# Optimization experiments

Measured on AMD Instinct MI355X. Metric: run time of the kernel, lower is better.

Reference implementation:

```python
import jax, jax.numpy as jnp
import numpy as np

D_MODEL = 1024
RANK = 256
INIT_ALPHA = 0.5


def setup_inputs() -> dict:
    key = jax.random.key(0)
    ks = jax.random.split(key, 12)
    D, R = D_MODEL, RANK
    s = 0.02
    return {
        "x": jax.random.normal(ks[0], (4, 2048, D), dtype=jnp.float32),
        "Wq": jax.random.normal(ks[1], (D, D), dtype=jnp.float32) * s,
        "Wk": jax.random.normal(ks[2], (D, D), dtype=jnp.float32) * s,
        "Wo": jax.random.normal(ks[3], (D, D), dtype=jnp.float32) * s,
        "U_b": jax.random.normal(ks[4], (D, R), dtype=jnp.float32) * s,
        "V_b": jax.random.normal(ks[5], (D, R), dtype=jnp.float32) * s,
        "W_b": jax.random.normal(ks[6], (D, R), dtype=jnp.float32) * s,
        "bias_b": jnp.zeros((D,), dtype=jnp.float32),
        "U_t": jax.random.normal(ks[7], (D, R), dtype=jnp.float32) * s,
        "V_t": jax.random.normal(ks[8], (D, R), dtype=jnp.float32) * s,
        "W_t": jax.random.normal(ks[9], (D, R), dtype=jnp.float32) * s,
        "X_t": jax.random.normal(ks[10], (D, R), dtype=jnp.float32) * s,
        "bias_t": jnp.zeros((D,), dtype=jnp.float32),
        "alpha": jnp.asarray(INIT_ALPHA, dtype=jnp.float32),
    }


def reference(x, Wq, Wk, Wo, U_b, V_b, W_b, bias_b, U_t, V_t, W_t, X_t, bias_t, alpha):
    # Math identical to the original O(T^2 D) materialization (attention_mask=None path),
    # reduced to causal cumulative sums: sum_{j<=i} (q_i * k_j) = q_i * cumsum_j(k_j).
    B, T, D = x.shape
    Q = x @ Wq.T                      # [B,T,D] (nn.Linear: x @ W^T)
    K = x @ Wk.T
    counts = jnp.arange(1, T + 1, dtype=x.dtype)[None, :, None]  # [1,T,1]
    Z = jnp.cumsum(x, axis=1) / counts  # causal cumulative mean [B,T,D]

    # Bilinear: sum_{j<=i} ((Q_i V_b) * (K_j W_b)) U_b^T + bias_b (per j)
    a_b = Q @ V_b                     # [B,T,R]
    c_b = jnp.cumsum(K @ W_b, axis=1) # [B,T,R] causal sum over j
    bil = (a_b * c_b) @ U_b.T         # [B,T,D]

    # Trilinear: sum_{j<=i} ((Q_i V_t) * (K_j W_t) * (Z_i X_t)) U_t^T + bias_t
    a_t = Q @ V_t
    c_t = jnp.cumsum(K @ W_t, axis=1)
    z_t = Z @ X_t
    tri = (a_t * z_t * c_t) @ U_t.T   # [B,T,D]

    # Per-i division by n_valid = i+1; the per-(i,j) biases average back to themselves.
    out = (bil + alpha * tri) / counts + (bias_b + alpha * bias_t)
    return out @ Wo.T                 # W_O (dropout=0 -> identity)
```

## Files before the change

kernel.cpp:

```cpp
#include <hip/hip_runtime.h>

#define NBATCH  4
#define TSEQ    2048
#define MROWS   8192
#define NCAT    1280
#define NE      512

#define OFF_WQT   0u
#define OFF_WKT   524288u
#define OFF_WOB   1048576u
#define OFF_VCT   1572864u
#define OFF_WCT   1835008u
#define OFF_UCT   2097152u
#define OFF_B2    2359296u
#define OFF_PB    2360320u
#define OFF_GB    3015680u
#define OFF_Y     3277824u
#define OFF_SCR   13763584u
#define OFF_XB    13861888u
#define OFF_EB    OFF_XB

typedef __attribute__((ext_vector_type(8))) short bf16x8;
typedef __attribute__((ext_vector_type(4))) float f32x4;

__device__ __forceinline__ unsigned short f2bf(float f) {
  union { float f; unsigned u; } v; v.f = f;
  return (unsigned short)((v.u + 0x7fff + ((v.u >> 16) & 1)) >> 16);
}

__device__ __forceinline__ void gload16(const void* g, void* l) {
  __builtin_amdgcn_global_load_lds(
      (const __attribute__((address_space(1))) unsigned*)g,
      (__attribute__((address_space(3))) unsigned*)l, 16, 0, 0);
}

template <int EPI, int OBF, int CS>
__device__ __forceinline__ void mfma_tile(
    const short* __restrict__ A, const short* __restrict__ B, void* __restrict__ Cv,
    int K, int ldA, int ldB, int ldC, int m0, int n0,
    const float* __restrict__ bias, float* __restrict__ scr, short* L) {
  const int tid = threadIdx.x;
  const int l = tid & 63;
  const int wv = tid >> 6;
  const int wm = (wv >> 1) * 64, wn = (wv & 1) * 64;
  const int sr = tid >> 2;
  const int sc4 = tid & 3;
  const int arow = wm + (l & 15), brow = wn + (l & 15);
  const int kq = l >> 4;

  f32x4 acc[4][4] = {};

#define STAGE(k0, par) do {                                                  \
    short* As_ = L + (par) * 8192;                                           \
    short* Bs_ = As_ + 4096;                                                 \
    _Pragma("unroll")                                                        \
    for (int p = 0; p < 2; ++p) {                                            \
      const int r = p * 64 + sr;                                             \
      const int sw = (sc4 ^ (r & 3)) * 8;                                    \
      gload16(A + (size_t)(m0 + r) * ldA + (k0) + sw, As_ + r * 32 + sc4 * 8); \
      gload16(B + (size_t)(n0 + r) * ldB + (k0) + sw, Bs_ + r * 32 + sc4 * 8); \
    }                                                                        \
  } while (0)

#define COMPUTE(par) do {                                                    \
    short* As_ = L + (par) * 8192;                                           \
    short* Bs_ = As_ + 4096;                                                 \
    bf16x8 af[4], bfr[4];                                                    \
    _Pragma("unroll")                                                        \
    for (int m = 0; m < 4; ++m) {                                            \
      const int r = arow + m * 16;                                           \
      af[m] = *(const bf16x8*)&As_[r * 32 + ((kq ^ (r & 3)) * 8)];           \
    }                                                                        \
    _Pragma("unroll")                                                        \
    for (int n = 0; n < 4; ++n) {                                            \
      const int r = brow + n * 16;                                           \
      bfr[n] = *(const bf16x8*)&Bs_[r * 32 + ((kq ^ (r & 3)) * 8)];          \
    }                                                                        \
    _Pragma("unroll")                                                        \
    for (int m = 0; m < 4; ++m)                                              \
      _Pragma("unroll")                                                      \
      for (int n = 0; n < 4; ++n)                                            \
        acc[m][n] = __builtin_amdgcn_mfma_f32_16x16x32_bf16(af[m], bfr[n], acc[m][n], 0, 0, 0); \
  } while (0)

  STAGE(0, 0);
  const int nt = K >> 5;
  for (int t = 0; t < nt; ++t) {
    if (t + 1 < nt) {
      STAGE((t + 1) << 5, (t + 1) & 1);
      asm volatile("s_waitcnt vmcnt(4)" ::: "memory");
    } else {
      asm volatile("s_waitcnt vmcnt(0)" ::: "memory");
    }
    asm volatile("s_barrier" ::: "memory");
    COMPUTE(t & 1);
    asm volatile("s_barrier" ::: "memory");
  }
#undef STAGE
#undef COMPUTE

  const int cc = wn + (l & 15);
  const int crb = wm + (l >> 4) * 4;
#pragma unroll
  for (int m = 0; m < 4; ++m) {
#pragma unroll
    for (int j = 0; j < 4; ++j) {
      const int gm = m0 + crb + m * 16 + j;
      float inv = 1.0f;
      if (EPI) inv = 1.0f / (float)((gm & (TSEQ - 1)) + 1);
#pragma unroll
      for (int n = 0; n < 4; ++n) {
        const int gn = n0 + cc + n * 16;
        float v = acc[m][n][j];
        if (EPI) v = v * inv + bias[gn];
        if (OBF) ((short*)Cv)[(size_t)gm * ldC + gn] = (short)f2bf(v);
        else     ((float*)Cv)[(size_t)gm * ldC + gn] = v;
      }
    }
  }
  if (CS && n0 >= 512) {
    const int bb = (m0 + wm) >> 11;
    const int seg = ((m0 + wm) & (TSEQ - 1)) >> 6;
    float* sp = scr + (size_t)(bb * 32 + seg) * 768 + (n0 - 512);
#pragma unroll
    for (int n = 0; n < 4; ++n) {
      float s = 0.f;
#pragma unroll
      for (int m = 0; m < 4; ++m)
#pragma unroll
        for (int j = 0; j < 4; ++j) s += acc[m][n][j];
      s += __shfl_xor(s, 16, 64);
      s += __shfl_xor(s, 32, 64);
      if (l < 16) sp[cc + n * 16] = s;
    }
  }
}

__device__ __forceinline__ void xcd_swizzle(int& bx, int& by) {
  const int gx = gridDim.x;
  const int nwg = gx * gridDim.y;
  const int n = by * gx + bx;
  const int q = nwg >> 3;
  const int s = (n & 7) * q + (n >> 3);
  bx = s % gx; by = s / gx;
}

template <int EPI, int CS>
__global__ __launch_bounds__(256) void mfma_nt(
    const short* __restrict__ A, const short* __restrict__ B,
    float* __restrict__ C, int K, int ldA, int ldB, int ldC,
    const float* __restrict__ bias, float* __restrict__ scr) {
  __shared__ short L[16384];
  int bx = blockIdx.x, by = blockIdx.y;
  xcd_swizzle(bx, by);
  mfma_tile<EPI, 0, CS>(A, B, C, K, ldA, ldB, ldC,
                        by * 128, bx * 128, bias, scr, L);
}

__global__ __launch_bounds__(256) void prep_mfma(
    const short* __restrict__ VCT, const short* __restrict__ WQT,
    const short* __restrict__ WCT, const short* __restrict__ WKT,
    const short* __restrict__ WOB, const short* __restrict__ UCT,
    short* __restrict__ Pb, short* __restrict__ Gb) {
  __shared__ short L[16384];
  const int g = blockIdx.x >> 5, t = blockIdx.x & 31;
  if (g == 0)
    mfma_tile<0, 1, 0>(VCT, WQT, Pb, 1024, 1024, 1024, 1024,
                       (t >> 3) * 128, (t & 7) * 128, nullptr, nullptr, L);
  else if (g == 1)
    mfma_tile<0, 1, 0>(WCT, WKT, Pb + (size_t)512 * 1024, 1024, 1024, 1024, 1024,
                       (t >> 3) * 128, (t & 7) * 128, nullptr, nullptr, L);
  else
    mfma_tile<0, 1, 0>(WOB, UCT, Gb, 1024, 1024, 1024, 512,
                       (t >> 2) * 128, (t & 3) * 128, nullptr, nullptr, L);
}

__global__ __launch_bounds__(256) void prep_all(
    const float* __restrict__ Vb, const float* __restrict__ Vt,
    const float* __restrict__ Wb, const float* __restrict__ Wt,
    const float* __restrict__ Ub, const float* __restrict__ Ut,
    const float* __restrict__ Xt, const float* __restrict__ Wq,
    const float* __restrict__ Wk, const float* __restrict__ Wo,
    const float* __restrict__ x,
    const float* __restrict__ bias_b, const float* __restrict__ bias_t,
    const float* __restrict__ alpha_p,
    short* __restrict__ VCT, short* __restrict__ WCT, short* __restrict__ UCT,
    short* __restrict__ PbXt, short* __restrict__ WQT, short* __restrict__ WKT,
    short* __restrict__ WOB, short* __restrict__ xb, float* __restrict__ b2) {
  const int bid = blockIdx.x;
  const int tid = threadIdx.x;
  if (bid >= 10176) {
    const float al = *alpha_p;
    const int d = bid - 10176;
    float s = 0.f;
    for (int e = tid; e < 1024; e += 256)
      s += Wo[(size_t)d * 1024 + e] * (bias_b[e] + al * bias_t[e]);
    __shared__ float red[256];
    red[tid] = s; __syncthreads();
    for (int off = 128; off > 0; off >>= 1) {
      if (tid < off) red[tid] += red[tid + off];
      __syncthreads();
    }
    if (tid == 0) b2[d] = red[0];
    return;
  }
  if (bid >= 960) {
    const size_t j = ((size_t)(bid - 960) * 256 + tid) * 4;
    const int isWo = j < 1048576u;
    const float* s = isWo ? &Wo[j] : &x[j - 1048576u];
    const float4 v = *(const float4*)s;
    ushort4 o;
    o.x = f2bf(v.x); o.y = f2bf(v.y); o.z = f2bf(v.z); o.w = f2bf(v.w);
    unsigned short* dst = (unsigned short*)(isWo ? WOB : xb);
    *(ushort4*)&dst[isWo ? j : j - 1048576u] = o;
    return;
  }
  const float* src; short* O; int r0, d0, c0, ldS;
  if (bid < 384) {
    const int z = bid >> 7, t = bid & 127;
    r0 = (t >> 4) * 64; d0 = (t & 15) * 64; ldS = 256;
    const float* S0 = z == 0 ? Vb : z == 1 ? Wb : Ub;
    const float* S1 = z == 0 ? Vt : z == 1 ? Wt : Ut;
    O = z == 0 ? VCT : z == 1 ? WCT : UCT;
    src = (r0 < 256) ? S0 : S1; c0 = r0 & 255;
  } else if (bid < 448) {
    const int t = bid - 384;
    r0 = (t >> 4) * 64; d0 = (t & 15) * 64; ldS = 256;
    src = Xt; c0 = r0; O = PbXt;
  } else {
    const int t = bid - 448;
    const int w = t >> 8, tt = t & 255;
    r0 = (tt >> 4) * 64; d0 = (tt & 15) * 64; ldS = 1024;
    src = w ? Wk : Wq; O = w ? WKT : WQT; c0 = r0;
  }
  __shared__ float Ts[64][65];
  const int lr = tid >> 4;
  const int lc = (tid & 15) * 4;
#pragma unroll
  for (int p = 0; p < 4; ++p) {
    const int row = lr + p * 16;
    const float4 v = *(const float4*)&src[(size_t)(d0 + row) * ldS + c0 + lc];
    Ts[row][lc + 0] = v.x; Ts[row][lc + 1] = v.y;
    Ts[row][lc + 2] = v.z; Ts[row][lc + 3] = v.w;
  }
  __syncthreads();
#pragma unroll
  for (int p = 0; p < 4; ++p) {
    const int ri = lr + p * 16;
    ushort4 o;
    o.x = f2bf(Ts[lc + 0][ri]); o.y = f2bf(Ts[lc + 1][ri]);
    o.z = f2bf(Ts[lc + 2][ri]); o.w = f2bf(Ts[lc + 3][ri]);
    *(ushort4*)&((unsigned short*)O)[(size_t)(r0 + ri) * 1024 + d0 + lc] = o;
  }
}

__global__ void cumsum_s2(float* __restrict__ scr) {
  const int lane = threadIdx.x;
  const int cg = blockIdx.x, b = blockIdx.z;
  const int c = cg * 64 + lane;
  float run = 0.f;
  for (int seg = 0; seg < 32; ++seg) {
    const size_t idx = (size_t)(b * 32 + seg) * 768 + c;
    const float v = scr[idx];
    scr[idx] = run;
    run += v;
  }
}

__global__ __launch_bounds__(256) void scan_combine(
    const float* __restrict__ Y, const float* __restrict__ scr,
    short* __restrict__ Eb, const float* __restrict__ alpha_p) {
  const float al = *alpha_p;
  const int c2 = threadIdx.x;
  const int seg = blockIdx.x, b = blockIdx.y;
  const float* sc = scr + (size_t)(b * 32 + seg) * 768;
  float run_cb = sc[c2];
  float run_ct = sc[256 + c2];
  float run_zt = sc[512 + c2];
  const size_t row0 = (size_t)(b * TSEQ + seg * 64);
  const float* yr = Y + row0 * NCAT;
  float ab = yr[c2], at = yr[256 + c2];
  float cb = yr[512 + c2], ct = yr[768 + c2], zt = yr[1024 + c2];
  for (int tt = 0; tt < 64; ++tt) {
    float nab = 0, nat = 0, ncb = 0, nct = 0, nzt = 0;
    if (tt < 63) {
      const float* yn = yr + NCAT;
      nab = yn[c2]; nat = yn[256 + c2];
      ncb = yn[512 + c2]; nct = yn[768 + c2]; nzt = yn[1024 + c2];
    }
    run_cb += cb; run_ct += ct; run_zt += zt;
    const float inv = 1.0f / (float)(seg * 64 + tt + 1);
    short* er = Eb + (row0 + tt) * 512;
    er[c2]       = (short)f2bf(ab * run_cb);
    er[256 + c2] = (short)f2bf(al * at * (run_zt * inv) * run_ct);
    ab = nab; at = nat; cb = ncb; ct = nct; zt = nzt;
    yr += NCAT;
  }
}

extern "C" void kernel_launch(void* const* d_in, const int* in_sizes, int n_in,
                              void* d_out, int out_size, void* d_ws, size_t ws_size,
                              hipStream_t stream) {
  const float* x      = (const float*)d_in[0];
  const float* Wq     = (const float*)d_in[1];
  const float* Wk     = (const float*)d_in[2];
  const float* Wo     = (const float*)d_in[3];
  const float* Ub     = (const float*)d_in[4];
  const float* Vb     = (const float*)d_in[5];
  const float* Wb     = (const float*)d_in[6];
  const float* bias_b = (const float*)d_in[7];
  const float* Ut     = (const float*)d_in[8];
  const float* Vt     = (const float*)d_in[9];
  const float* Wt     = (const float*)d_in[10];
  const float* Xt     = (const float*)d_in[11];
  const float* bias_t = (const float*)d_in[12];
  const float* alpha  = (const float*)d_in[13];
  float* out = (float*)d_out;
  float* ws  = (float*)d_ws;

  short* WQT = (short*)(ws + OFF_WQT);
  short* WKT = (short*)(ws + OFF_WKT);
  short* WOB = (short*)(ws + OFF_WOB);
  short* VCT = (short*)(ws + OFF_VCT);
  short* WCT = (short*)(ws + OFF_WCT);
  short* UCT = (short*)(ws + OFF_UCT);
  float* b2  = ws + OFF_B2;
  short* Pb  = (short*)(ws + OFF_PB);
  short* Gb  = (short*)(ws + OFF_GB);
  float* Y   = ws + OFF_Y;
  float* scr = ws + OFF_SCR;
  short* xb  = (short*)(ws + OFF_XB);
  short* Eb  = (short*)(ws + OFF_EB);

  prep_all<<<11200, 256, 0, stream>>>(Vb, Vt, Wb, Wt, Ub, Ut, Xt, Wq, Wk, Wo, x,
                                      bias_b, bias_t, alpha,
                                      VCT, WCT, UCT, Pb + (size_t)1024 * 1024,
                                      WQT, WKT, WOB, xb, b2);
  prep_mfma<<<96, 256, 0, stream>>>(VCT, WQT, WCT, WKT, WOB, UCT, Pb, Gb);
  mfma_nt<0, 1><<<dim3(NCAT / 128, MROWS / 128), 256, 0, stream>>>(
      xb, Pb, Y, 1024, 1024, 1024, NCAT, nullptr, scr);
  cumsum_s2<<<dim3(12, 1, NBATCH), 64, 0, stream>>>(scr);
  scan_combine<<<dim3(32, NBATCH), 256, 0, stream>>>(Y, scr, Eb, alpha);
  mfma_nt<1, 0><<<dim3(1024 / 128, MROWS / 128), 256, 0, stream>>>(
      Eb, Gb, out, 512, 512, 512, 1024, b2, nullptr);
}
```

Measured before the change: 203.3 us.

## Triple-buffer GEMM LDS pipeline, store Y in bf16, unroll scan with prefetch

The shared MFMA tile loop moves from double to triple buffering in LDS, so global loads run two k-steps ahead. The first GEMM now writes its intermediate Y in bf16 rather than fp32, which halves that write and the matching read in scan_combine. scan_combine is unrolled eight rows deep with register prefetch to hide load latency in the serial scan. The costs are 50% more LDS per block, which may lower occupancy, and extra rounding error from storing Y in bf16 before the cumulative sums.

```diff
diff --git a/kernel.cpp b/kernel.cpp
--- a/kernel.cpp
+++ b/kernel.cpp
@@ -27,6 +27,10 @@
   union { float f; unsigned u; } v; v.f = f;
   return (unsigned short)((v.u + 0x7fff + ((v.u >> 16) & 1)) >> 16);
 }
+__device__ __forceinline__ float bf2f(unsigned short u) {
+  union { unsigned u; float f; } v; v.u = ((unsigned)u) << 16;
+  return v.f;
+}
 
 __device__ __forceinline__ void gload16(const void* g, void* l) {
   __builtin_amdgcn_global_load_lds(
@@ -50,8 +54,8 @@
 
   f32x4 acc[4][4] = {};
 
-#define STAGE(k0, par) do {                                                  \
-    short* As_ = L + (par) * 8192;                                           \
+#define STAGE(k0, buf) do {                                                  \
+    short* As_ = L + (buf) * 8192;                                           \
     short* Bs_ = As_ + 4096;                                                 \
     _Pragma("unroll")                                                        \
     for (int p = 0; p < 2; ++p) {                                            \
@@ -62,8 +66,8 @@
     }                                                                        \
   } while (0)
 
-#define COMPUTE(par) do {                                                    \
-    short* As_ = L + (par) * 8192;                                           \
+#define COMPUTE(buf) do {                                                    \
+    short* As_ = L + (buf) * 8192;                                           \
     short* Bs_ = As_ + 4096;                                                 \
     bf16x8 af[4], bfr[4];                                                    \
     _Pragma("unroll")                                                        \
@@ -84,17 +88,23 @@
   } while (0)
 
   STAGE(0, 0);
+  STAGE(32, 1);
   const int nt = K >> 5;
+  int cur = 0, nxt = 2;
   for (int t = 0; t < nt; ++t) {
-    if (t + 1 < nt) {
-      STAGE((t + 1) << 5, (t + 1) & 1);
+    if (t + 2 < nt) {
+      STAGE((t + 2) << 5, nxt);
+      asm volatile("s_waitcnt vmcnt(8)" ::: "memory");
+    } else if (t + 1 < nt) {
       asm volatile("s_waitcnt vmcnt(4)" ::: "memory");
     } else {
       asm volatile("s_waitcnt vmcnt(0)" ::: "memory");
     }
     asm volatile("s_barrier" ::: "memory");
-    COMPUTE(t & 1);
+    COMPUTE(cur);
     asm volatile("s_barrier" ::: "memory");
+    cur = (cur == 2) ? 0 : cur + 1;
+    nxt = (nxt == 2) ? 0 : nxt + 1;
   }
 #undef STAGE
 #undef COMPUTE
@@ -145,16 +155,16 @@
   bx = s % gx; by = s / gx;
 }
 
-template <int EPI, int CS>
+template <int EPI, int OBF, int CS>
 __global__ __launch_bounds__(256) void mfma_nt(
     const short* __restrict__ A, const short* __restrict__ B,
-    float* __restrict__ C, int K, int ldA, int ldB, int ldC,
+    void* __restrict__ C, int K, int ldA, int ldB, int ldC,
     const float* __restrict__ bias, float* __restrict__ scr) {
-  __shared__ short L[16384];
+  __shared__ short L[24576];
   int bx = blockIdx.x, by = blockIdx.y;
   xcd_swizzle(bx, by);
-  mfma_tile<EPI, 0, CS>(A, B, C, K, ldA, ldB, ldC,
-                        by * 128, bx * 128, bias, scr, L);
+  mfma_tile<EPI, OBF, CS>(A, B, C, K, ldA, ldB, ldC,
+                          by * 128, bx * 128, bias, scr, L);
 }
 
 __global__ __launch_bounds__(256) void prep_mfma(
@@ -162,7 +172,7 @@
     const short* __restrict__ WCT, const short* __restrict__ WKT,
     const short* __restrict__ WOB, const short* __restrict__ UCT,
     short* __restrict__ Pb, short* __restrict__ Gb) {
-  __shared__ short L[16384];
+  __shared__ short L[24576];
   const int g = blockIdx.x >> 5, t = blockIdx.x & 31;
   if (g == 0)
     mfma_tile<0, 1, 0>(VCT, WQT, Pb, 1024, 1024, 1024, 1024,
@@ -267,36 +277,49 @@
   }
 }
 
+#define LOADR(s, t) {                                                   \
+    const unsigned short* p_ = yb + (size_t)(t) * NCAT;                 \
+    ab##s = bf2f(p_[c2]);        at##s = bf2f(p_[256 + c2]);            \
+    cb##s = bf2f(p_[512 + c2]);  ct##s = bf2f(p_[768 + c2]);            \
+    zt##s = bf2f(p_[1024 + c2]); }
+#define STEPR(s, t) {                                                   \
+    run_cb += cb##s; run_ct += ct##s; run_zt += zt##s;                  \
+    const float inv_ = 1.0f / (float)(segbase + (t) + 1);               \
+    unsigned short* er_ = Eb + (row0 + (t)) * 512;                      \
+    er_[c2]       = f2bf(ab##s * run_cb);                               \
+    er_[256 + c2] = f2bf(al * at##s * (run_zt * inv_) * run_ct); }
 __global__ __launch_bounds__(256) void scan_combine(
-    const float* __restrict__ Y, const float* __restrict__ scr,
-    short* __restrict__ Eb, const float* __restrict__ alpha_p) {
+    const unsigned short* __restrict__ Y, const float* __restrict__ scr,
+    unsigned short* __restrict__ Eb, const float* __restrict__ alpha_p) {
   const float al = *alpha_p;
   const int c2 = threadIdx.x;
   const int seg = blockIdx.x, b = blockIdx.y;
+  const int segbase = seg * 64;
   const float* sc = scr + (size_t)(b * 32 + seg) * 768;
   float run_cb = sc[c2];
   float run_ct = sc[256 + c2];
   float run_zt = sc[512 + c2];
-  const size_t row0 = (size_t)(b * TSEQ + seg * 64);
-  const float* yr = Y + row0 * NCAT;
-  float ab = yr[c2], at = yr[256 + c2];
-  float cb = yr[512 + c2], ct = yr[768 + c2], zt = yr[1024 + c2];
-  for (int tt = 0; tt < 64; ++tt) {
-    float nab = 0, nat = 0, ncb = 0, nct = 0, nzt = 0;
-    if (tt < 63) {
-      const float* yn = yr + NCAT;
-      nab = yn[c2]; nat = yn[256 + c2];
-      ncb = yn[512 + c2]; nct = yn[768 + c2]; nzt = yn[1024 + c2];
-    }
-    run_cb += cb; run_ct += ct; run_zt += zt;
-    const float inv = 1.0f / (float)(seg * 64 + tt + 1);
-    short* er = Eb + (row0 + tt) * 512;
-    er[c2]       = (short)f2bf(ab * run_cb);
-    er[256 + c2] = (short)f2bf(al * at * (run_zt * inv) * run_ct);
-    ab = nab; at = nat; cb = ncb; ct = nct; zt = nzt;
-    yr += NCAT;
-  }
-}
+  const size_t row0 = (size_t)(b * TSEQ + segbase);
+  const unsigned short* yb = Y + row0 * NCAT;
+  float ab0, at0, cb0, ct0, zt0, ab1, at1, cb1, ct1, zt1;
+  float ab2, at2, cb2, ct2, zt2, ab3, at3, cb3, ct3, zt3;
+  float ab4, at4, cb4, ct4, zt4, ab5, at5, cb5, ct5, zt5;
+  float ab6, at6, cb6, ct6, zt6, ab7, at7, cb7, ct7, zt7;
+  LOADR(0, 0) LOADR(1, 1) LOADR(2, 2) LOADR(3, 3)
+  LOADR(4, 4) LOADR(5, 5) LOADR(6, 6) LOADR(7, 7)
+  for (int t = 0; t < 64; t += 8) {
+    STEPR(0, t + 0) if (t + 8 < 64)  LOADR(0, t + 8)
+    STEPR(1, t + 1) if (t + 9 < 64)  LOADR(1, t + 9)
+    STEPR(2, t + 2) if (t + 10 < 64) LOADR(2, t + 10)
+    STEPR(3, t + 3) if (t + 11 < 64) LOADR(3, t + 11)
+    STEPR(4, t + 4) if (t + 12 < 64) LOADR(4, t + 12)
+    STEPR(5, t + 5) if (t + 13 < 64) LOADR(5, t + 13)
+    STEPR(6, t + 6) if (t + 14 < 64) LOADR(6, t + 14)
+    STEPR(7, t + 7) if (t + 15 < 64) LOADR(7, t + 15)
+  }
+}
+#undef LOADR
+#undef STEPR
 
 extern "C" void kernel_launch(void* const* d_in, const int* in_sizes, int n_in,
                               void* d_out, int out_size, void* d_ws, size_t ws_size,
@@ -327,7 +350,7 @@
   float* b2  = ws + OFF_B2;
   short* Pb  = (short*)(ws + OFF_PB);
   short* Gb  = (short*)(ws + OFF_GB);
-  float* Y   = ws + OFF_Y;
+  unsigned short* Yb = (unsigned short*)(ws + OFF_Y);
   float* scr = ws + OFF_SCR;
   short* xb  = (short*)(ws + OFF_XB);
   short* Eb  = (short*)(ws + OFF_EB);
@@ -337,10 +360,10 @@
                                       VCT, WCT, UCT, Pb + (size_t)1024 * 1024,
                                       WQT, WKT, WOB, xb, b2);
   prep_mfma<<<96, 256, 0, stream>>>(VCT, WQT, WCT, WKT, WOB, UCT, Pb, Gb);
-  mfma_nt<0, 1><<<dim3(NCAT / 128, MROWS / 128), 256, 0, stream>>>(
-      xb, Pb, Y, 1024, 1024, 1024, NCAT, nullptr, scr);
+  mfma_nt<0, 1, 1><<<dim3(NCAT / 128, MROWS / 128), 256, 0, stream>>>(
+      xb, Pb, Yb, 1024, 1024, 1024, NCAT, nullptr, scr);
   cumsum_s2<<<dim3(12, 1, NBATCH), 64, 0, stream>>>(scr);
-  scan_combine<<<dim3(32, NBATCH), 256, 0, stream>>>(Y, scr, Eb, alpha);
-  mfma_nt<1, 0><<<dim3(1024 / 128, MROWS / 128), 256, 0, stream>>>(
+  scan_combine<<<dim3(32, NBATCH), 256, 0, stream>>>(Yb, scr, (unsigned short*)Eb, alpha);
+  mfma_nt<1, 0, 0><<<dim3(1024 / 128, MROWS / 128), 256, 0, stream>>>(
       Eb, Gb, out, 512, 512, 512, 1024, b2, nullptr);
 }
```

After: 204.1 us. Within noise of the previous version (+0.4%).
